# Performance work log

Measured on AMD Instinct MI355X. Metric: run time of the kernel, lower is better.

The kernel has to match this reference:

```python
import jax, jax.numpy as jnp
import numpy as np

EMBED = 512
NH = 8
HD = EMBED // NH
NL = 12
FFN = 2048
TD = 16  # latent_channels * patch_size**2 = 4*4


def _ln(x, g, b):
    m = x.mean(-1, keepdims=True)
    v = ((x - m) ** 2).mean(-1, keepdims=True)
    return (x - m) * jax.lax.rsqrt(v + 1e-5) * g + b


def _pos_emb(H, W, d):
    # faithful to get_2d_rope_embedding: cosine 1D embeddings along h and w, concatenated
    dh = d // 2
    inv = 1.0 / (10000.0 ** (jnp.arange(dh, dtype=jnp.float32) / dh))
    peh = jnp.cos(jnp.arange(H, dtype=jnp.float32)[:, None] * inv[None, :])  # (H, dh)
    pew = jnp.cos(jnp.arange(W, dtype=jnp.float32)[:, None] * inv[None, :])  # (W, dh)
    pe = jnp.concatenate([
        jnp.broadcast_to(peh[:, None, :], (H, W, dh)),
        jnp.broadcast_to(pew[None, :, :], (H, W, dh)),
    ], axis=-1)
    return pe.reshape(H * W, d)


def setup_inputs() -> dict:
    key = jax.random.key(0)
    ks = jax.random.split(key, 20)
    B, L = 8, 1024
    s = 0.02
    inp = {
        'x': jax.random.normal(ks[0], (B, L, TD), jnp.float32),
        'token_mask': jnp.ones((B, L), jnp.int32),
        'W_in': s * jax.random.normal(ks[1], (TD, EMBED), jnp.float32),
        'b_in': jnp.zeros((EMBED,), jnp.float32),
        'ln1_g': jnp.ones((NL, EMBED), jnp.float32),
        'ln1_b': jnp.zeros((NL, EMBED), jnp.float32),
        'Wq': s * jax.random.normal(ks[2], (NL, EMBED, EMBED), jnp.float32),
        'Wk': s * jax.random.normal(ks[3], (NL, EMBED, EMBED), jnp.float32),
        'Wv': s * jax.random.normal(ks[4], (NL, EMBED, EMBED), jnp.float32),
        'Wo': s * jax.random.normal(ks[5], (NL, EMBED, EMBED), jnp.float32),
        'ln2_g': jnp.ones((NL, EMBED), jnp.float32),
        'ln2_b': jnp.zeros((NL, EMBED), jnp.float32),
        'W1': s * jax.random.normal(ks[6], (NL, EMBED, FFN), jnp.float32),
        'W2': s * jax.random.normal(ks[7], (NL, EMBED, FFN), jnp.float32),
        'W3': s * jax.random.normal(ks[8], (NL, FFN, EMBED), jnp.float32),
        'W_out': s * jax.random.normal(ks[9], (EMBED, TD), jnp.float32),
        'b_out': jnp.zeros((TD,), jnp.float32),
        'H': 32,
        'W': 32,
    }
    return inp


def reference(x, token_mask, W_in, b_in, ln1_g, ln1_b, Wq, Wk, Wv, Wo,
              ln2_g, ln2_b, W1, W2, W3, W_out, b_out, H, W):
    B, L, _ = x.shape
    scale = 1.0 / np.sqrt(HD).astype(np.float32)
    h = x @ W_in + b_in + _pos_emb(H, W, EMBED)[None]  # (B, L, E)
    # (B,1,1,L) additive mask, -1e9 at padded positions
    mask = (token_mask == 0)[:, None, None, :].astype(h.dtype) * (-1e9)

    def block(h, p):
        g1, b1, wq, wk, wv, wo, g2, b2, w1, w2, w3 = p
        xn = _ln(h, g1, b1)
        q = (xn @ wq).reshape(B, L, NH, HD)
        k = (xn @ wk).reshape(B, L, NH, HD)
        v = (xn @ wv).reshape(B, L, NH, HD)
        s = jnp.einsum('blhd,bmhd->bhlm', q, k) * scale + mask
        a = jax.nn.softmax(s, axis=-1)
        o = jnp.einsum('bhlm,bmhd->blhd', a, v).reshape(B, L, EMBED) @ wo
        h = h + o
        xn = _ln(h, g2, b2)
        h = h + (jax.nn.silu(xn @ w1) * (xn @ w2)) @ w3
        return h, None

    h, _ = jax.lax.scan(block, h, (ln1_g, ln1_b, Wq, Wk, Wv, Wo, ln2_g, ln2_b, W1, W2, W3))
    return h @ W_out + b_out  # (B, L, TD)
```

## Files before the change

### kernel.cpp

```cpp
#include <hip/hip_runtime.h>

typedef __attribute__((ext_vector_type(8))) short short8;
typedef __attribute__((ext_vector_type(4))) float f32x4;
typedef __attribute__((ext_vector_type(4))) unsigned short us4;

#define MFMA_BF16(a,b,c) __builtin_amdgcn_mfma_f32_16x16x32_bf16((a),(b),(c),0,0,0)

__device__ __forceinline__ unsigned short f2bf(float f) {
  unsigned int u = __float_as_uint(f);
  u += 0x7fffu + ((u >> 16) & 1u);
  return (unsigned short)(u >> 16);
}

__device__ __forceinline__ unsigned cvt_pk_bf16(float lo, float hi) {
  unsigned r;
  asm("v_cvt_pk_bf16_f32 %0, %1, %2" : "=v"(r) : "v"(lo), "v"(hi));
  return r;
}

__device__ __forceinline__ int xcd_swz(int lid, int nwg) {
  return (lid & 7) * (nwg >> 3) + (lid >> 3);
}

__global__ __launch_bounds__(256) void wtrans_kernel(const float* __restrict__ src,
                                                     unsigned short* __restrict__ dst,
                                                     int R, int C) {
  __shared__ float tile[32][33];
  int c0 = blockIdx.x * 32, r0 = blockIdx.y * 32;
  const float* s = src + (size_t)blockIdx.z * R * C;
  unsigned short* d = dst + (size_t)blockIdx.z * R * C;
  int tx = threadIdx.x, ty = threadIdx.y;
#pragma unroll
  for (int i = 0; i < 32; i += 8)
    tile[ty + i][tx] = s[(size_t)(r0 + ty + i) * C + c0 + tx];
  __syncthreads();
#pragma unroll
  for (int i = 0; i < 32; i += 8)
    d[(size_t)(c0 + ty + i) * R + r0 + tx] = f2bf(tile[tx][ty + i]);
}

__global__ __launch_bounds__(128) void embed_kernel(const float* __restrict__ x,
                                                    const float* __restrict__ Win,
                                                    const float* __restrict__ bin,
                                                    float* __restrict__ h) {
  __shared__ float xs[16];
  int m = blockIdx.x, t = threadIdx.x;
  if (t < 16) xs[t] = x[m * 16 + t];
  __syncthreads();
  int l = m & 1023, hi = l >> 5, wi = l & 31;
#pragma unroll
  for (int e0 = 0; e0 < 512; e0 += 128) {
    int e = e0 + t;
    float a = bin[e];
#pragma unroll
    for (int kk = 0; kk < 16; kk++) a += xs[kk] * Win[kk * 512 + e];
    int j = e & 255;
    float p = (e < 256) ? (float)hi : (float)wi;
    float inv = expf((float)j * (-9.210340371976184f / 256.0f));
    a += cosf(p * inv);
    h[(size_t)m * 512 + e] = a;
  }
}

__global__ __launch_bounds__(256) void ln_kernel(const float* __restrict__ h,
                                                 const float* __restrict__ gw,
                                                 const float* __restrict__ bw,
                                                 unsigned short* __restrict__ xn) {
  int row = blockIdx.x * 4 + (threadIdx.x >> 6);
  int lane = threadIdx.x & 63;
  const f32x4* hr = (const f32x4*)&h[(size_t)row * 512];
  f32x4 v0 = hr[lane], v1 = hr[lane + 64];
  float s = v0[0]+v0[1]+v0[2]+v0[3] + v1[0]+v1[1]+v1[2]+v1[3];
  float q = v0[0]*v0[0]+v0[1]*v0[1]+v0[2]*v0[2]+v0[3]*v0[3]
          + v1[0]*v1[0]+v1[1]*v1[1]+v1[2]*v1[2]+v1[3]*v1[3];
#pragma unroll
  for (int o = 1; o < 64; o <<= 1) { s += __shfl_xor(s, o); q += __shfl_xor(q, o); }
  float mean = s * (1.0f / 512.0f);
  float var = q * (1.0f / 512.0f) - mean * mean;
  float rstd = rsqrtf(var + 1e-5f);
  f32x4 g0 = ((const f32x4*)gw)[lane], g1 = ((const f32x4*)gw)[lane + 64];
  f32x4 b0 = ((const f32x4*)bw)[lane], b1 = ((const f32x4*)bw)[lane + 64];
  us4 w0, w1;
#pragma unroll
  for (int r = 0; r < 4; r++) {
    w0[r] = f2bf((v0[r] - mean) * rstd * g0[r] + b0[r]);
    w1[r] = f2bf((v1[r] - mean) * rstd * g1[r] + b1[r]);
  }
  *(us4*)&xn[(size_t)row * 512 + lane * 4] = w0;
  *(us4*)&xn[(size_t)row * 512 + 256 + lane * 4] = w1;
}

__global__ __launch_bounds__(512) void qkv_gemm(const unsigned short* __restrict__ xn,
                                                const unsigned short* __restrict__ wtq,
                                                const unsigned short* __restrict__ wtk,
                                                const unsigned short* __restrict__ wtv,
                                                unsigned short* __restrict__ qo,
                                                unsigned short* __restrict__ ko,
                                                unsigned short* __restrict__ vt) {
  __shared__ short8 As[2048];
  __shared__ short8 Bs[1024];
  int n0 = blockIdx.x * 128, m0 = blockIdx.y * 256;
  int sel = n0 >> 9;
  const short8* wt = (const short8*)(sel == 0 ? wtq : sel == 1 ? wtk : wtv);
  int nw = n0 & 511;
  const short8* A8 = (const short8*)xn;
  int tid = threadIdx.x, wid = tid >> 6, lane = tid & 63;
  int wr = wid >> 1, wc = wid & 1, c16 = lane & 15, g = lane >> 4;
  const short8* aSrc[4];
  const short8* bSrc[2];
#pragma unroll
  for (int s = 0; s < 4; s++) {
    int sub = wid * 4 + s, rg = sub >> 1, kc = sub & 1;
    aSrc[s] = A8 + (size_t)(m0 + rg * 16 + c16) * 64 + kc * 4 + g;
  }
#pragma unroll
  for (int s = 0; s < 2; s++) {
    int sub = wid * 2 + s, rg = sub >> 1, kc = sub & 1;
    bSrc[s] = wt + (size_t)(nw + rg * 16 + c16) * 64 + kc * 4 + g;
  }
  f32x4 acc[4][4] = {};
  short8 ra[4], rb[2];
#pragma unroll
  for (int s = 0; s < 4; s++) ra[s] = aSrc[s][0];
#pragma unroll
  for (int s = 0; s < 2; s++) rb[s] = bSrc[s][0];
  for (int kt = 0; kt < 8; kt++) {
    __syncthreads();
#pragma unroll
    for (int s = 0; s < 4; s++) As[(wid * 4 + s) * 64 + lane] = ra[s];
#pragma unroll
    for (int s = 0; s < 2; s++) Bs[(wid * 2 + s) * 64 + lane] = rb[s];
    if (kt < 7) {
#pragma unroll
      for (int s = 0; s < 4; s++) ra[s] = aSrc[s][(kt + 1) * 8];
#pragma unroll
      for (int s = 0; s < 2; s++) rb[s] = bSrc[s][(kt + 1) * 8];
    }
    __syncthreads();
#pragma unroll
    for (int kc = 0; kc < 2; kc++) {
      short8 af[4], bf[4];
#pragma unroll
      for (int mf = 0; mf < 4; mf++) af[mf] = As[((wr * 4 + mf) * 2 + kc) * 64 + lane];
#pragma unroll
      for (int nf = 0; nf < 4; nf++) bf[nf] = Bs[((wc * 4 + nf) * 2 + kc) * 64 + lane];
#pragma unroll
      for (int mf = 0; mf < 4; mf++)
#pragma unroll
        for (int nf = 0; nf < 4; nf++)
          acc[mf][nf] = MFMA_BF16(af[mf], bf[nf], acc[mf][nf]);
    }
  }
  if (sel < 2) {
    unsigned short* out = sel == 0 ? qo : ko;
#pragma unroll
    for (int mf = 0; mf < 4; mf++)
#pragma unroll
      for (int nf = 0; nf < 4; nf++) {
        int col = nw + wc * 64 + nf * 16 + c16;
#pragma unroll
        for (int r = 0; r < 4; r++) {
          int row = m0 + wr * 64 + mf * 16 + g * 4 + r;
          out[(size_t)row * 512 + col] = f2bf(acc[mf][nf][r]);
        }
      }
  } else {
    int b8 = (m0 >> 10) * 8;
    int loff = (m0 & 1023) + wr * 64;
#pragma unroll
    for (int mf = 0; mf < 4; mf++)
#pragma unroll
      for (int nf = 0; nf < 4; nf++) {
        int c = nw + wc * 64 + nf * 16 + c16;
        int bh = b8 + (c >> 6), d = c & 63;
        us4 w;
#pragma unroll
        for (int r = 0; r < 4; r++) w[r] = f2bf(acc[mf][nf][r]);
        *(us4*)&vt[(size_t)(bh * 64 + d) * 1024 + loff + mf * 16 + g * 4] = w;
      }
  }
}

__global__ __launch_bounds__(512) void gemm_res(const unsigned short* __restrict__ A,
                                                const unsigned short* __restrict__ Wt,
                                                float* __restrict__ h, int Kd8, int nkt64) {
  __shared__ short8 As[1024];
  __shared__ short8 Bs[1024];
  int n0 = blockIdx.x * 128, m0 = blockIdx.y * 128;
  const short8* A8 = (const short8*)A;
  const short8* W8 = (const short8*)Wt;
  int tid = threadIdx.x, wid = tid >> 6, lane = tid & 63;
  int wr = wid >> 2, wc = wid & 3, c16 = lane & 15, g = lane >> 4;
  const short8* aSrc[2];
  const short8* bSrc[2];
#pragma unroll
  for (int s = 0; s < 2; s++) {
    int sub = wid * 2 + s, rg = sub >> 1, kc = sub & 1;
    aSrc[s] = A8 + (size_t)(m0 + rg * 16 + c16) * Kd8 + kc * 4 + g;
    bSrc[s] = W8 + (size_t)(n0 + rg * 16 + c16) * Kd8 + kc * 4 + g;
  }
  f32x4 acc[4][2] = {};
  short8 ra[2], rb[2];
#pragma unroll
  for (int s = 0; s < 2; s++) { ra[s] = aSrc[s][0]; rb[s] = bSrc[s][0]; }
  for (int kt = 0; kt < nkt64; kt++) {
    __syncthreads();
#pragma unroll
    for (int s = 0; s < 2; s++) {
      As[(wid * 2 + s) * 64 + lane] = ra[s];
      Bs[(wid * 2 + s) * 64 + lane] = rb[s];
    }
    if (kt + 1 < nkt64) {
#pragma unroll
      for (int s = 0; s < 2; s++) {
        ra[s] = aSrc[s][(kt + 1) * 8];
        rb[s] = bSrc[s][(kt + 1) * 8];
      }
    }
    __syncthreads();
#pragma unroll
    for (int kc = 0; kc < 2; kc++) {
      short8 af[4], bf[2];
#pragma unroll
      for (int mf = 0; mf < 4; mf++) af[mf] = As[((wr * 4 + mf) * 2 + kc) * 64 + lane];
#pragma unroll
      for (int nf = 0; nf < 2; nf++) bf[nf] = Bs[((wc * 2 + nf) * 2 + kc) * 64 + lane];
#pragma unroll
      for (int mf = 0; mf < 4; mf++)
#pragma unroll
        for (int nf = 0; nf < 2; nf++)
          acc[mf][nf] = MFMA_BF16(af[mf], bf[nf], acc[mf][nf]);
    }
  }
#pragma unroll
  for (int mf = 0; mf < 4; mf++)
#pragma unroll
    for (int nf = 0; nf < 2; nf++) {
      int col = n0 + wc * 32 + nf * 16 + c16;
#pragma unroll
      for (int r = 0; r < 4; r++) {
        int row = m0 + wr * 64 + mf * 16 + g * 4 + r;
        h[(size_t)row * 512 + col] += acc[mf][nf][r];
      }
    }
}

__global__ __launch_bounds__(512) void ffn_gemm(const unsigned short* __restrict__ xn,
                                                const unsigned short* __restrict__ w1t,
                                                const unsigned short* __restrict__ w2t,
                                                unsigned short* __restrict__ gout) {
  __shared__ short8 As[2048];
  __shared__ short8 B1s[1024];
  __shared__ short8 B2s[1024];
  int n0 = blockIdx.x * 128, m0 = blockIdx.y * 256;
  const short8* A8 = (const short8*)xn;
  const short8* W18 = (const short8*)w1t;
  const short8* W28 = (const short8*)w2t;
  int tid = threadIdx.x, wid = tid >> 6, lane = tid & 63;
  int wr = wid >> 1, wc = wid & 1, c16 = lane & 15, g = lane >> 4;
  const short8* aSrc[4];
  const short8* b1Src[2];
  const short8* b2Src[2];
#pragma unroll
  for (int s = 0; s < 4; s++) {
    int sub = wid * 4 + s, rg = sub >> 1, kc = sub & 1;
    aSrc[s] = A8 + (size_t)(m0 + rg * 16 + c16) * 64 + kc * 4 + g;
  }
#pragma unroll
  for (int s = 0; s < 2; s++) {
    int sub = wid * 2 + s, rg = sub >> 1, kc = sub & 1;
    b1Src[s] = W18 + (size_t)(n0 + rg * 16 + c16) * 64 + kc * 4 + g;
    b2Src[s] = W28 + (size_t)(n0 + rg * 16 + c16) * 64 + kc * 4 + g;
  }
  f32x4 acc1[4][4] = {};
  f32x4 acc2[4][4] = {};
  short8 ra[4], rb1[2], rb2[2];
#pragma unroll
  for (int s = 0; s < 4; s++) ra[s] = aSrc[s][0];
#pragma unroll
  for (int s = 0; s < 2; s++) { rb1[s] = b1Src[s][0]; rb2[s] = b2Src[s][0]; }
  for (int kt = 0; kt < 8; kt++) {
    __syncthreads();
#pragma unroll
    for (int s = 0; s < 4; s++) As[(wid * 4 + s) * 64 + lane] = ra[s];
#pragma unroll
    for (int s = 0; s < 2; s++) {
      B1s[(wid * 2 + s) * 64 + lane] = rb1[s];
      B2s[(wid * 2 + s) * 64 + lane] = rb2[s];
    }
    if (kt < 7) {
#pragma unroll
      for (int s = 0; s < 4; s++) ra[s] = aSrc[s][(kt + 1) * 8];
#pragma unroll
      for (int s = 0; s < 2; s++) {
        rb1[s] = b1Src[s][(kt + 1) * 8];
        rb2[s] = b2Src[s][(kt + 1) * 8];
      }
    }
    __syncthreads();
#pragma unroll
    for (int kc = 0; kc < 2; kc++) {
      short8 af[4], b1f[4], b2f[4];
#pragma unroll
      for (int mf = 0; mf < 4; mf++) af[mf] = As[((wr * 4 + mf) * 2 + kc) * 64 + lane];
#pragma unroll
      for (int nf = 0; nf < 4; nf++) {
        b1f[nf] = B1s[((wc * 4 + nf) * 2 + kc) * 64 + lane];
        b2f[nf] = B2s[((wc * 4 + nf) * 2 + kc) * 64 + lane];
      }
#pragma unroll
      for (int mf = 0; mf < 4; mf++)
#pragma unroll
        for (int nf = 0; nf < 4; nf++) {
          acc1[mf][nf] = MFMA_BF16(af[mf], b1f[nf], acc1[mf][nf]);
          acc2[mf][nf] = MFMA_BF16(af[mf], b2f[nf], acc2[mf][nf]);
        }
    }
  }
#pragma unroll
  for (int mf = 0; mf < 4; mf++)
#pragma unroll
    for (int nf = 0; nf < 4; nf++) {
      int col = n0 + wc * 64 + nf * 16 + c16;
#pragma unroll
      for (int r = 0; r < 4; r++) {
        int row = m0 + wr * 64 + mf * 16 + g * 4 + r;
        float xx = acc1[mf][nf][r];
        float yy = acc2[mf][nf][r];
        float sg = xx / (1.0f + __expf(-xx));
        gout[(size_t)row * 2048 + col] = f2bf(sg * yy);
      }
    }
}

__global__ __launch_bounds__(256) void attn_kernel(const unsigned short* __restrict__ q,
                                                   const unsigned short* __restrict__ k,
                                                   const unsigned short* __restrict__ vt,
                                                   const int* __restrict__ tmsk,
                                                   unsigned short* __restrict__ o) {
  __shared__ short8 Ks[512];
  __shared__ short8 Vs[512];
  __shared__ uint2  Pb[2048];
  __shared__ f32x4  maskv[256];

  int s = xcd_swz((int)blockIdx.x, 512);
  int qb = s & 7;
  int bh = s >> 3;
  int b = bh >> 3, hh = bh & 7;
  int tid = threadIdx.x, wid = tid >> 6, lane = tid & 63;
  int c16 = lane & 15, gq = lane >> 4;
  int qrow0 = qb * 128 + wid * 32;

  const short8* q8 = (const short8*)q;
  const short8* k8 = (const short8*)k;
  const short8* v8 = (const short8*)vt;

  short8 qf[2][2];
#pragma unroll
  for (int nf = 0; nf < 2; nf++)
#pragma unroll
    for (int dc = 0; dc < 2; dc++)
      qf[nf][dc] = q8[(size_t)(b * 1024 + qrow0 + nf * 16 + c16) * 64 + hh * 8 + dc * 4 + gq];

  {
    int4 mm = ((const int4*)(tmsk + b * 1024))[tid];
    f32x4 ma;
    ma[0] = (mm.x == 0) ? -1.442695e9f : 0.0f;
    ma[1] = (mm.y == 0) ? -1.442695e9f : 0.0f;
    ma[2] = (mm.z == 0) ? -1.442695e9f : 0.0f;
    ma[3] = (mm.w == 0) ? -1.442695e9f : 0.0f;
    maskv[tid] = ma;
  }

  short8 rk[2], rv[2];
#pragma unroll
  for (int ss = 0; ss < 2; ss++) {
    int sub = wid * 2 + ss;
    rk[ss] = k8[(size_t)(b * 1024 + (sub >> 1) * 16 + c16) * 64 + hh * 8 + (sub & 1) * 4 + gq];
    rv[ss] = v8[(size_t)(bh * 64 + (sub >> 1) * 16 + c16) * 128 + (sub & 1) * 4 + gq];
  }

  float mrun[2] = {-1e30f, -1e30f};
  float lrun[2] = {0.0f, 0.0f};
  f32x4 accO[4][2] = {};
  const float SCL = 0.125f * 1.4426950408889634f;

  for (int kt = 0; kt < 16; kt++) {
    __syncthreads();
#pragma unroll
    for (int ss = 0; ss < 2; ss++) {
      int sub = wid * 2 + ss;
      Ks[sub * 64 + lane] = rk[ss];
      Vs[sub * 64 + lane] = rv[ss];
    }
    if (kt < 15) {
      int kt2 = kt + 1;
#pragma unroll
      for (int ss = 0; ss < 2; ss++) {
        int sub = wid * 2 + ss;
        rk[ss] = k8[(size_t)(b * 1024 + kt2 * 64 + (sub >> 1) * 16 + c16) * 64 + hh * 8 + (sub & 1) * 4 + gq];
        rv[ss] = v8[(size_t)(bh * 64 + (sub >> 1) * 16 + c16) * 128 + kt2 * 8 + (sub & 1) * 4 + gq];
      }
    }
    __syncthreads();

    f32x4 sT[4][2] = {};
    __builtin_amdgcn_s_setprio(1);
#pragma unroll
    for (int mf = 0; mf < 4; mf++) {
      short8 ka0 = Ks[(mf * 2 + 0) * 64 + lane];
      short8 ka1 = Ks[(mf * 2 + 1) * 64 + lane];
#pragma unroll
      for (int nf = 0; nf < 2; nf++) {
        sT[mf][nf] = MFMA_BF16(ka0, qf[nf][0], sT[mf][nf]);
        sT[mf][nf] = MFMA_BF16(ka1, qf[nf][1], sT[mf][nf]);
      }
    }
    __builtin_amdgcn_s_setprio(0);

#pragma unroll
    for (int nf = 0; nf < 2; nf++) {
      float pv[4][4];
      float tm = -1e30f;
#pragma unroll
      for (int mf = 0; mf < 4; mf++) {
        f32x4 mk = maskv[kt * 16 + mf * 4 + gq];
#pragma unroll
        for (int r = 0; r < 4; r++) {
          float sv = sT[mf][nf][r] * SCL + mk[r];
          pv[mf][r] = sv;
          tm = fmaxf(tm, sv);
        }
      }
      tm = fmaxf(tm, __shfl_xor(tm, 16));
      tm = fmaxf(tm, __shfl_xor(tm, 32));
      if (!__all(tm - mrun[nf] <= 8.0f)) {
        float mn = fmaxf(mrun[nf], tm);
        float fac = exp2f(mrun[nf] - mn);
        mrun[nf] = mn;
        lrun[nf] *= fac;
#pragma unroll
        for (int dmf = 0; dmf < 4; dmf++) accO[dmf][nf] *= fac;
      }
      float ts = 0.0f;
#pragma unroll
      for (int mf = 0; mf < 4; mf++)
#pragma unroll
        for (int r = 0; r < 4; r++) {
          float p = exp2f(pv[mf][r] - mrun[nf]);
          pv[mf][r] = p;
          ts += p;
        }
      ts += __shfl_xor(ts, 16);
      ts += __shfl_xor(ts, 32);
      lrun[nf] += ts;
#pragma unroll
      for (int mf = 0; mf < 4; mf++) {
        unsigned lo = cvt_pk_bf16(pv[mf][0], pv[mf][1]);
        unsigned hi = cvt_pk_bf16(pv[mf][2], pv[mf][3]);
        int kk = mf >> 1;
        int gr = (mf & 1) * 2 + (gq >> 1);
        uint2 t2; t2.x = lo; t2.y = hi;
        Pb[wid * 512 + ((nf * 2 + kk) * 64 + gr * 16 + c16) * 2 + (gq & 1)] = t2;
      }
    }

    const short8* Pb8 = (const short8*)Pb;
    __builtin_amdgcn_s_setprio(1);
#pragma unroll
    for (int nf = 0; nf < 2; nf++) {
      short8 pb0 = Pb8[wid * 256 + (nf * 2 + 0) * 64 + lane];
      short8 pb1 = Pb8[wid * 256 + (nf * 2 + 1) * 64 + lane];
#pragma unroll
      for (int dmf = 0; dmf < 4; dmf++) {
        short8 va0 = Vs[(dmf * 2 + 0) * 64 + lane];
        short8 va1 = Vs[(dmf * 2 + 1) * 64 + lane];
        accO[dmf][nf] = MFMA_BF16(va0, pb0, accO[dmf][nf]);
        accO[dmf][nf] = MFMA_BF16(va1, pb1, accO[dmf][nf]);
      }
    }
    __builtin_amdgcn_s_setprio(0);
  }

#pragma unroll
  for (int nf = 0; nf < 2; nf++) {
    float inv = 1.0f / lrun[nf];
    int row = b * 1024 + qrow0 + nf * 16 + c16;
#pragma unroll
    for (int dmf = 0; dmf < 4; dmf++) {
      us4 w;
#pragma unroll
      for (int r = 0; r < 4; r++) w[r] = f2bf(accO[dmf][nf][r] * inv);
      *(us4*)&o[(size_t)row * 512 + hh * 64 + dmf * 16 + gq * 4] = w;
    }
  }
}

__global__ __launch_bounds__(128) void out_kernel(const float* __restrict__ h,
                                                  const float* __restrict__ Wout,
                                                  const float* __restrict__ bout,
                                                  float* __restrict__ out) {
  __shared__ f32x4 hs4[8][128];
  __shared__ f32x4 Ws4[16][129];
  int t = threadIdx.x;
  int rb = blockIdx.x * 8;
  float* hsf = (float*)hs4;
  float* wsf = (float*)Ws4;
  for (int i = t; i < 4096; i += 128) hsf[i] = h[(size_t)rb * 512 + i];
  for (int i = t; i < 8192; i += 128) wsf[(i & 15) * 516 + (i >> 4)] = Wout[i];
  __syncthreads();
  int r = t >> 4, c = t & 15;
  float acc = bout[c];
  for (int k4 = 0; k4 < 128; k4++) {
    f32x4 a = hs4[r][k4];
    f32x4 w = Ws4[c][k4];
    acc += a[0]*w[0] + a[1]*w[1] + a[2]*w[2] + a[3]*w[3];
  }
  out[(rb + r) * 16 + c] = acc;
}

extern "C" void kernel_launch(void* const* d_in, const int* in_sizes, int n_in,
                              void* d_out, int out_size, void* d_ws, size_t ws_size,
                              hipStream_t stream) {
  const float* x    = (const float*)d_in[0];
  const int*   tmsk = (const int*)d_in[1];
  const float* Win  = (const float*)d_in[2];
  const float* bin  = (const float*)d_in[3];
  const float* ln1g = (const float*)d_in[4];
  const float* ln1b = (const float*)d_in[5];
  const float* Wq   = (const float*)d_in[6];
  const float* Wk   = (const float*)d_in[7];
  const float* Wv   = (const float*)d_in[8];
  const float* Wo   = (const float*)d_in[9];
  const float* ln2g = (const float*)d_in[10];
  const float* ln2b = (const float*)d_in[11];
  const float* W1   = (const float*)d_in[12];
  const float* W2   = (const float*)d_in[13];
  const float* W3   = (const float*)d_in[14];
  const float* Wout = (const float*)d_in[15];
  const float* bout = (const float*)d_in[16];
  float* outp = (float*)d_out;

  char* ws = (char*)d_ws;
  unsigned short* wtq = (unsigned short*)(ws + 0);
  unsigned short* wtk = (unsigned short*)(ws + 6291456);
  unsigned short* wtv = (unsigned short*)(ws + 12582912);
  unsigned short* wto = (unsigned short*)(ws + 18874368);
  unsigned short* wt1 = (unsigned short*)(ws + 25165824);
  unsigned short* wt2 = (unsigned short*)(ws + 50331648);
  unsigned short* wt3 = (unsigned short*)(ws + 75497472);
  float*          h   = (float*)(ws + 100663296);
  unsigned short* xn  = (unsigned short*)(ws + 117440512);
  unsigned short* qb  = (unsigned short*)(ws + 125829120);
  unsigned short* kb  = (unsigned short*)(ws + 134217728);
  unsigned short* vtb = (unsigned short*)(ws + 150994944);
  unsigned short* ob  = (unsigned short*)(ws + 159383552);
  unsigned short* gb  = (unsigned short*)(ws + 167772160);

  dim3 tb(32, 8);
  wtrans_kernel<<<dim3(16, 16, 12), tb, 0, stream>>>(Wq, wtq, 512, 512);
  wtrans_kernel<<<dim3(16, 16, 12), tb, 0, stream>>>(Wk, wtk, 512, 512);
  wtrans_kernel<<<dim3(16, 16, 12), tb, 0, stream>>>(Wv, wtv, 512, 512);
  wtrans_kernel<<<dim3(16, 16, 12), tb, 0, stream>>>(Wo, wto, 512, 512);
  wtrans_kernel<<<dim3(64, 16, 12), tb, 0, stream>>>(W1, wt1, 512, 2048);
  wtrans_kernel<<<dim3(64, 16, 12), tb, 0, stream>>>(W2, wt2, 512, 2048);
  wtrans_kernel<<<dim3(16, 64, 12), tb, 0, stream>>>(W3, wt3, 2048, 512);

  embed_kernel<<<8192, 128, 0, stream>>>(x, Win, bin, h);

  for (int l = 0; l < 12; l++) {
    ln_kernel<<<2048, 256, 0, stream>>>(h, ln1g + l * 512, ln1b + l * 512, xn);
    qkv_gemm<<<dim3(12, 32), 512, 0, stream>>>(xn,
        wtq + (size_t)l * 262144, wtk + (size_t)l * 262144, wtv + (size_t)l * 262144,
        qb, kb, vtb);
    attn_kernel<<<512, 256, 0, stream>>>(qb, kb, vtb, tmsk, ob);
    gemm_res<<<dim3(4, 64), 512, 0, stream>>>(ob, wto + (size_t)l * 262144, h, 64, 8);
    ln_kernel<<<2048, 256, 0, stream>>>(h, ln2g + l * 512, ln2b + l * 512, xn);
    ffn_gemm<<<dim3(16, 32), 512, 0, stream>>>(xn,
        wt1 + (size_t)l * 1048576, wt2 + (size_t)l * 1048576, gb);
    gemm_res<<<dim3(4, 64), 512, 0, stream>>>(gb, wt3 + (size_t)l * 1048576, h, 256, 32);
  }
  out_kernel<<<1024, 128, 0, stream>>>(h, Wout, bout, outp);

  (void)in_sizes; (void)n_in; (void)out_size; (void)ws_size;
}
```

Measured before the change: 2.267 ms.

## Double-buffer LDS tiles in residual and FFN GEMMs with single barrier per step

Switches gemm_res and ffn_gemm to double-buffered shared-memory tiles. The next K tile is written into the alternate buffer while MFMAs consume the current one, so each iteration needs one barrier instead of two. In ffn_gemm the K step shrinks from 64 to 32, doubling the iteration count while keeping LDS size constant and lowering prefetch register pressure. The cost is more iterations, and therefore more barriers, for the FFN kernel.

After: 2.271 ms. About the same (+0.1%).

```diff
diff --git a/kernel.cpp b/kernel.cpp
--- a/kernel.cpp
+++ b/kernel.cpp
@@ -184,8 +184,8 @@
 __global__ __launch_bounds__(512) void gemm_res(const unsigned short* __restrict__ A,
                                                 const unsigned short* __restrict__ Wt,
                                                 float* __restrict__ h, int Kd8, int nkt64) {
-  __shared__ short8 As[1024];
-  __shared__ short8 Bs[1024];
+  __shared__ short8 As[2][1024];
+  __shared__ short8 Bs[2][1024];
   int n0 = blockIdx.x * 128, m0 = blockIdx.y * 128;
   const short8* A8 = (const short8*)A;
   const short8* W8 = (const short8*)Wt;
@@ -203,34 +203,46 @@
   short8 ra[2], rb[2];
 #pragma unroll
   for (int s = 0; s < 2; s++) { ra[s] = aSrc[s][0]; rb[s] = bSrc[s][0]; }
+#pragma unroll
+  for (int s = 0; s < 2; s++) {
+    As[0][(wid * 2 + s) * 64 + lane] = ra[s];
+    Bs[0][(wid * 2 + s) * 64 + lane] = rb[s];
+  }
+  if (nkt64 > 1) {
+#pragma unroll
+    for (int s = 0; s < 2; s++) { ra[s] = aSrc[s][8]; rb[s] = bSrc[s][8]; }
+  }
+  __syncthreads();
   for (int kt = 0; kt < nkt64; kt++) {
-    __syncthreads();
-#pragma unroll
-    for (int s = 0; s < 2; s++) {
-      As[(wid * 2 + s) * 64 + lane] = ra[s];
-      Bs[(wid * 2 + s) * 64 + lane] = rb[s];
-    }
+    int cur = kt & 1;
     if (kt + 1 < nkt64) {
 #pragma unroll
       for (int s = 0; s < 2; s++) {
-        ra[s] = aSrc[s][(kt + 1) * 8];
-        rb[s] = bSrc[s][(kt + 1) * 8];
-      }
-    }
-    __syncthreads();
+        As[cur ^ 1][(wid * 2 + s) * 64 + lane] = ra[s];
+        Bs[cur ^ 1][(wid * 2 + s) * 64 + lane] = rb[s];
+      }
+      if (kt + 2 < nkt64) {
+#pragma unroll
+        for (int s = 0; s < 2; s++) {
+          ra[s] = aSrc[s][(kt + 2) * 8];
+          rb[s] = bSrc[s][(kt + 2) * 8];
+        }
+      }
+    }
 #pragma unroll
     for (int kc = 0; kc < 2; kc++) {
       short8 af[4], bf[2];
 #pragma unroll
-      for (int mf = 0; mf < 4; mf++) af[mf] = As[((wr * 4 + mf) * 2 + kc) * 64 + lane];
-#pragma unroll
-      for (int nf = 0; nf < 2; nf++) bf[nf] = Bs[((wc * 2 + nf) * 2 + kc) * 64 + lane];
+      for (int mf = 0; mf < 4; mf++) af[mf] = As[cur][((wr * 4 + mf) * 2 + kc) * 64 + lane];
+#pragma unroll
+      for (int nf = 0; nf < 2; nf++) bf[nf] = Bs[cur][((wc * 2 + nf) * 2 + kc) * 64 + lane];
 #pragma unroll
       for (int mf = 0; mf < 4; mf++)
 #pragma unroll
         for (int nf = 0; nf < 2; nf++)
           acc[mf][nf] = MFMA_BF16(af[mf], bf[nf], acc[mf][nf]);
     }
+    __syncthreads();
   }
 #pragma unroll
   for (int mf = 0; mf < 4; mf++)
@@ -249,73 +261,69 @@
                                                 const unsigned short* __restrict__ w1t,
                                                 const unsigned short* __restrict__ w2t,
                                                 unsigned short* __restrict__ gout) {
-  __shared__ short8 As[2048];
-  __shared__ short8 B1s[1024];
-  __shared__ short8 B2s[1024];
+  __shared__ short8 As[2][1024];
+  __shared__ short8 B1s[2][512];
+  __shared__ short8 B2s[2][512];
   int n0 = blockIdx.x * 128, m0 = blockIdx.y * 256;
   const short8* A8 = (const short8*)xn;
   const short8* W18 = (const short8*)w1t;
   const short8* W28 = (const short8*)w2t;
   int tid = threadIdx.x, wid = tid >> 6, lane = tid & 63;
   int wr = wid >> 1, wc = wid & 1, c16 = lane & 15, g = lane >> 4;
-  const short8* aSrc[4];
-  const short8* b1Src[2];
-  const short8* b2Src[2];
-#pragma unroll
-  for (int s = 0; s < 4; s++) {
-    int sub = wid * 4 + s, rg = sub >> 1, kc = sub & 1;
-    aSrc[s] = A8 + (size_t)(m0 + rg * 16 + c16) * 64 + kc * 4 + g;
-  }
+  const short8* aSrc[2];
+  const short8* b1Src;
+  const short8* b2Src;
 #pragma unroll
   for (int s = 0; s < 2; s++) {
-    int sub = wid * 2 + s, rg = sub >> 1, kc = sub & 1;
-    b1Src[s] = W18 + (size_t)(n0 + rg * 16 + c16) * 64 + kc * 4 + g;
-    b2Src[s] = W28 + (size_t)(n0 + rg * 16 + c16) * 64 + kc * 4 + g;
-  }
+    int sub = wid * 2 + s;
+    aSrc[s] = A8 + (size_t)(m0 + sub * 16 + c16) * 64 + g;
+  }
+  b1Src = W18 + (size_t)(n0 + wid * 16 + c16) * 64 + g;
+  b2Src = W28 + (size_t)(n0 + wid * 16 + c16) * 64 + g;
   f32x4 acc1[4][4] = {};
   f32x4 acc2[4][4] = {};
-  short8 ra[4], rb1[2], rb2[2];
-#pragma unroll
-  for (int s = 0; s < 4; s++) ra[s] = aSrc[s][0];
-#pragma unroll
-  for (int s = 0; s < 2; s++) { rb1[s] = b1Src[s][0]; rb2[s] = b2Src[s][0]; }
-  for (int kt = 0; kt < 8; kt++) {
+  short8 ra[2], rb1, rb2;
+#pragma unroll
+  for (int s = 0; s < 2; s++) ra[s] = aSrc[s][0];
+  rb1 = b1Src[0]; rb2 = b2Src[0];
+#pragma unroll
+  for (int s = 0; s < 2; s++) As[0][(wid * 2 + s) * 64 + lane] = ra[s];
+  B1s[0][wid * 64 + lane] = rb1;
+  B2s[0][wid * 64 + lane] = rb2;
+#pragma unroll
+  for (int s = 0; s < 2; s++) ra[s] = aSrc[s][4];
+  rb1 = b1Src[4]; rb2 = b2Src[4];
+  __syncthreads();
+  for (int kt = 0; kt < 16; kt++) {
+    int cur = kt & 1;
+    if (kt < 15) {
+#pragma unroll
+      for (int s = 0; s < 2; s++) As[cur ^ 1][(wid * 2 + s) * 64 + lane] = ra[s];
+      B1s[cur ^ 1][wid * 64 + lane] = rb1;
+      B2s[cur ^ 1][wid * 64 + lane] = rb2;
+      if (kt < 14) {
+#pragma unroll
+        for (int s = 0; s < 2; s++) ra[s] = aSrc[s][(kt + 2) * 4];
+        rb1 = b1Src[(kt + 2) * 4];
+        rb2 = b2Src[(kt + 2) * 4];
+      }
+    }
+    short8 af[4], b1f[4], b2f[4];
+#pragma unroll
+    for (int mf = 0; mf < 4; mf++) af[mf] = As[cur][(wr * 4 + mf) * 64 + lane];
+#pragma unroll
+    for (int nf = 0; nf < 4; nf++) {
+      b1f[nf] = B1s[cur][(wc * 4 + nf) * 64 + lane];
+      b2f[nf] = B2s[cur][(wc * 4 + nf) * 64 + lane];
+    }
+#pragma unroll
+    for (int mf = 0; mf < 4; mf++)
+#pragma unroll
+      for (int nf = 0; nf < 4; nf++) {
+        acc1[mf][nf] = MFMA_BF16(af[mf], b1f[nf], acc1[mf][nf]);
+        acc2[mf][nf] = MFMA_BF16(af[mf], b2f[nf], acc2[mf][nf]);
+      }
     __syncthreads();
-#pragma unroll
-    for (int s = 0; s < 4; s++) As[(wid * 4 + s) * 64 + lane] = ra[s];
-#pragma unroll
-    for (int s = 0; s < 2; s++) {
-      B1s[(wid * 2 + s) * 64 + lane] = rb1[s];
-      B2s[(wid * 2 + s) * 64 + lane] = rb2[s];
-    }
-    if (kt < 7) {
-#pragma unroll
-      for (int s = 0; s < 4; s++) ra[s] = aSrc[s][(kt + 1) * 8];
-#pragma unroll
-      for (int s = 0; s < 2; s++) {
-        rb1[s] = b1Src[s][(kt + 1) * 8];
-        rb2[s] = b2Src[s][(kt + 1) * 8];
-      }
-    }
-    __syncthreads();
-#pragma unroll
-    for (int kc = 0; kc < 2; kc++) {
-      short8 af[4], b1f[4], b2f[4];
-#pragma unroll
-      for (int mf = 0; mf < 4; mf++) af[mf] = As[((wr * 4 + mf) * 2 + kc) * 64 + lane];
-#pragma unroll
-      for (int nf = 0; nf < 4; nf++) {
-        b1f[nf] = B1s[((wc * 4 + nf) * 2 + kc) * 64 + lane];
-        b2f[nf] = B2s[((wc * 4 + nf) * 2 + kc) * 64 + lane];
-      }
-#pragma unroll
-      for (int mf = 0; mf < 4; mf++)
-#pragma unroll
-        for (int nf = 0; nf < 4; nf++) {
-          acc1[mf][nf] = MFMA_BF16(af[mf], b1f[nf], acc1[mf][nf]);
-          acc2[mf][nf] = MFMA_BF16(af[mf], b2f[nf], acc2[mf][nf]);
-        }
-    }
   }
 #pragma unroll
   for (int mf = 0; mf < 4; mf++)
```
